# Performance work log

Measured on AMD Instinct MI355X. Metric: run time of the kernel, lower is better.

The kernel has to match this reference:

```python
import jax, jax.numpy as jnp
import numpy as np

H_GRID = 24
W_GRID = 24
NUM_HEADS = 3
FEAT_DIM = 192
HEAD_DIM = FEAT_DIM // NUM_HEADS  # 64
SCALE = HEAD_DIM ** -0.5
LN_EPS = 1e-5


def _positional():
    # matches get_positional_encodings with intrinsics=None; depends only on grid
    ys = jnp.linspace(-1.0, 1.0, H_GRID)
    xs = jnp.linspace(-1.0, 1.0, W_GRID)
    p3 = jnp.tile(ys, W_GRID)            # [N]
    p4 = jnp.repeat(xs, H_GRID)          # [N]
    p2 = p3 * p4
    p1 = p4 * p4
    p0 = p3 * p3
    return jnp.stack([p0, p1, p2, p3, p4, jnp.ones_like(p0)], axis=1)  # [N, 6]


def _layernorm(x, w, b):
    mu = jnp.mean(x, axis=-1, keepdims=True)
    var = jnp.mean((x - mu) ** 2, axis=-1, keepdims=True)
    return (x - mu) / jnp.sqrt(var + LN_EPS) * w + b


def _qkv_heads(x, qkv_w):
    # x: [B, N, C] -> q,k,v each [B, H, N, hd]
    B, N, _ = x.shape
    qkv = x @ qkv_w.T                                    # [B, N, 3*F]
    qkv = qkv.reshape(B, N, 3, NUM_HEADS, HEAD_DIM)
    qkv = jnp.transpose(qkv, (2, 0, 3, 1, 4))            # [3, B, H, N, hd]
    return qkv[0], qkv[1], qkv[2]


def _dual_softmax(attn):
    return jax.nn.softmax(attn, axis=-1) * jax.nn.softmax(attn, axis=-2)


def setup_inputs() -> dict:
    key = jax.random.key(0)
    ks = jax.random.split(key, 4)
    B, C = 64, 256
    in_dim, out_dim = C, 512
    dim_size = 2 * NUM_HEADS * (HEAD_DIM + 6) * (HEAD_DIM + 6)  # 29400
    return {
        "x1": jax.random.normal(ks[0], (B, C, H_GRID, W_GRID), jnp.float32),
        "x2": jax.random.normal(ks[1], (B, C, H_GRID, W_GRID), jnp.float32),
        "ln_w": jnp.ones((in_dim,), jnp.float32),
        "ln_b": jnp.zeros((in_dim,), jnp.float32),
        "qkv_w": jax.random.normal(ks[2], (3 * FEAT_DIM, in_dim), jnp.float32) * (in_dim ** -0.5),
        "proj_w": jax.random.normal(ks[3], (out_dim, dim_size), jnp.float32) * (dim_size ** -0.5),
        "proj_b": jnp.zeros((out_dim,), jnp.float32),
    }


def reference(x1, x2, ln_w, ln_b, qkv_w, proj_w, proj_b):
    B, C, h, w = x1.shape
    N = h * w
    x1t = _layernorm(x1.reshape(B, C, N).transpose(0, 2, 1), ln_w, ln_b)  # [B, N, C]
    x2t = _layernorm(x2.reshape(B, C, N).transpose(0, 2, 1), ln_w, ln_b)

    q1, k1, v1 = _qkv_heads(x1t, qkv_w)
    q2, k2, v2 = _qkv_heads(x2t, qkv_w)

    attn_1 = jnp.einsum("bhnd,bhmd->bhnm", q2, k1) * SCALE
    attn_2 = jnp.einsum("bhnd,bhmd->bhnm", q1, k2) * SCALE
    af1 = _dual_softmax(attn_1)
    af2 = _dual_softmax(attn_2)

    pos = jnp.broadcast_to(_positional(), (B, NUM_HEADS, N, 6))
    v1p = jnp.concatenate([v1, pos], axis=-1)  # [B, H, N, hd+6]
    v2p = jnp.concatenate([v2, pos], axis=-1)

    f1 = jnp.einsum("bhnd,bhnm,bhme->bhde", v1p, af1, v1p)  # [B, H, hd+6, hd+6]
    f2 = jnp.einsum("bhnd,bhnm,bhme->bhde", v2p, af2, v2p)

    feat = jnp.concatenate([f1.reshape(B, -1), f2.reshape(B, -1)], axis=-1)
    return jax.nn.relu(feat @ proj_w.T + proj_b)
```

## Files before the change

kernel.cpp:

```cpp
#include <hip/hip_runtime.h>

#define NSEQ 576
#define CDIM 256
#define HEADS 3
#define HD 64
#define FEAT 192
#define QKVF 576
#define QK_F 384
#define VP 70
#define BHN 192
#define DIMSZ 29400

typedef __attribute__((ext_vector_type(8))) _Float16 half8;
typedef __attribute__((ext_vector_type(4))) _Float16 half4;
typedef __attribute__((ext_vector_type(4))) float f32x4;

#define MFMA16(A,B,C) __builtin_amdgcn_mfma_f32_16x16x32_f16(A,B,C,0,0,0)

__device__ __forceinline__ float posval(int n, int pe){
  int yi = n % 24, xi = n / 24;
  float py = (float)yi * (2.0f/23.0f) - 1.0f;
  float px = (float)xi * (2.0f/23.0f) - 1.0f;
  switch(pe){
    case 0: return py*py;
    case 1: return px*px;
    case 2: return py*px;
    case 3: return py;
    case 4: return px;
    default: return 1.0f;
  }
}

template<int LD>
__device__ __forceinline__ half8 fragT(const _Float16 (*s)[LD], int row, int dbase){
  half4 a = *(const half4*)&s[row][dbase];
  half4 b = *(const half4*)&s[row][dbase + 16];
  return __builtin_shufflevector(a, b, 0, 1, 2, 3, 4, 5, 6, 7);
}

__device__ __forceinline__ void stage_copy64(const _Float16* __restrict__ src, int rstr,
                                             _Float16 (*d)[72], int t){
  #pragma unroll
  for (int k2 = 0; k2 < 2; ++k2){
    int idx = t + 256 * k2;
    int row = idx >> 3, c = (idx & 7) << 3;
    half8 v = *(const half8*)(src + (size_t)row * rstr + c);
    *(half4*)&d[row][c]     = (half4){v[0], v[1], v[2], v[3]};
    *(half4*)&d[row][c + 4] = (half4){v[4], v[5], v[6], v[7]};
  }
}

__device__ __forceinline__ int rotIdx(int row, int c16){
  return row * 64 + ((((c16) + row) & 7) << 3);
}

__global__ __launch_bounds__(192) void k_ln_stats(const float* __restrict__ x1, const float* __restrict__ x2,
                                                  float* __restrict__ mu, float* __restrict__ rstd){
  int idx = blockIdx.x;
  int i2 = idx / 192;
  int rem = idx % 192;
  int b = rem / 3, ng = rem % 3;
  int n = ng * 192 + threadIdx.x;
  const float* x = i2 ? x2 : x1;
  const float* xb = x + (size_t)b * CDIM * NSEQ + n;
  float s = 0.f, sq = 0.f;
  for (int c = 0; c < CDIM; ++c){
    float v = xb[(size_t)c * NSEQ];
    s += v; sq += v * v;
  }
  float m = s * (1.0f/256.0f);
  float var = sq * (1.0f/256.0f) - m * m;
  int o = (i2 * 64 + b) * NSEQ + n;
  mu[o] = m;
  rstd[o] = rsqrtf(var + 1e-5f);
}

__global__ __launch_bounds__(256) void k_qkv_gemm_mfma(const float* __restrict__ x1, const float* __restrict__ x2,
                                                       const float* __restrict__ mu, const float* __restrict__ rstd,
                                                       const float* __restrict__ lnw, const float* __restrict__ lnb,
                                                       const float* __restrict__ qkvw,
                                                       _Float16* __restrict__ qh, _Float16* __restrict__ ql,
                                                       _Float16* __restrict__ vpTh, _Float16* __restrict__ vpTl){
  int wg = (blockIdx.x & 7) * 1296 + (blockIdx.x >> 3);
  int ft = wg % 9;
  int mt = wg / 9;
  int ibn = mt * 64;
  int i2 = ibn / (64 * NSEQ);
  int bn = ibn % (64 * NSEQ);
  int b  = bn / NSEQ;
  int n0 = bn % NSEQ;
  const float* x = i2 ? x2 : x1;
  const float* xb = x + (size_t)b * CDIM * NSEQ + n0;
  __shared__ __align__(16) _Float16 Xh[64][68];
  __shared__ __align__(16) _Float16 Xl[64][68];
  __shared__ __align__(16) _Float16 Wh[64][68];
  __shared__ __align__(16) _Float16 Wl[64][68];
  __shared__ float smu[64], srstd[64], slnw[256], slnb[256];
  int t = threadIdx.x;
  int w = t >> 6, lane = t & 63, tx = lane & 15, hi = lane >> 4;
  if (t < 64){ smu[t] = mu[ibn + t]; srstd[t] = rstd[ibn + t]; }
  slnw[t] = lnw[t]; slnb[t] = lnb[t];

  f32x4 acc[4];
  #pragma unroll
  for (int s = 0; s < 4; ++s) acc[s] = (f32x4){0.f, 0.f, 0.f, 0.f};

  int nA = t & 63, cg = t >> 6;
  int fr = t >> 2, cq = t & 3;
  for (int c0 = 0; c0 < CDIM; c0 += 64){
    __syncthreads();
    float mun = smu[nA], rsn = srstd[nA];
    #pragma unroll
    for (int rr = 0; rr < 16; ++rr){
      int c = cg * 16 + rr;
      float v = xb[(size_t)(c0 + c) * NSEQ + nA];
      float xv = (v - mun) * rsn * slnw[c0 + c] + slnb[c0 + c];
      _Float16 hh = (_Float16)xv;
      Xh[nA][c] = hh;
      Xl[nA][c] = (_Float16)(xv - (float)hh);
    }
    const float* wp = qkvw + (size_t)(ft * 64 + fr) * CDIM + c0 + cq * 16;
    #pragma unroll
    for (int rr = 0; rr < 4; ++rr){
      float4 wv = *(const float4*)(wp + rr * 4);
      half4 h, l;
      h.x = (_Float16)wv.x; l.x = (_Float16)(wv.x - (float)h.x);
      h.y = (_Float16)wv.y; l.y = (_Float16)(wv.y - (float)h.y);
      h.z = (_Float16)wv.z; l.z = (_Float16)(wv.z - (float)h.z);
      h.w = (_Float16)wv.w; l.w = (_Float16)(wv.w - (float)h.w);
      *(half4*)&Wh[fr][cq * 16 + rr * 4] = h;
      *(half4*)&Wl[fr][cq * 16 + rr * 4] = l;
    }
    __syncthreads();
    #pragma unroll
    for (int kc = 0; kc < 2; ++kc){
      half8 wh = fragT<68>(Wh, w * 16 + tx, kc * 32 + hi * 4);
      half8 wl = fragT<68>(Wl, w * 16 + tx, kc * 32 + hi * 4);
      #pragma unroll
      for (int s = 0; s < 4; ++s){
        half8 xh = fragT<68>(Xh, s * 16 + tx, kc * 32 + hi * 4);
        half8 xl = fragT<68>(Xl, s * 16 + tx, kc * 32 + hi * 4);
        acc[s] = MFMA16(xh, wh, acc[s]);
        acc[s] = MFMA16(xl, wh, acc[s]);
        acc[s] = MFMA16(xh, wl, acc[s]);
      }
    }
  }
  if (ft < 6){
    #pragma unroll
    for (int s = 0; s < 4; ++s)
      #pragma unroll
      for (int rr = 0; rr < 4; ++rr){
        float v = acc[s][rr];
        _Float16 hh = (_Float16)v;
        size_t o = (size_t)(ibn + s * 16 + hi * 4 + rr) * QK_F + ft * 64 + w * 16 + tx;
        qh[o] = hh;
        ql[o] = (_Float16)(v - (float)hh);
      }
  } else {
    __syncthreads();
    #pragma unroll
    for (int s = 0; s < 4; ++s)
      #pragma unroll
      for (int rr = 0; rr < 4; ++rr){
        float v = acc[s][rr];
        _Float16 hh = (_Float16)v;
        Xh[s * 16 + hi * 4 + rr][w * 16 + tx] = hh;
        Xl[s * 16 + hi * 4 + rr][w * 16 + tx] = (_Float16)(v - (float)hh);
      }
    __syncthreads();
    int mbg = i2 * 192 + b * 3 + (ft - 6);
    #pragma unroll
    for (int it = 0; it < 16; ++it){
      int d = (t >> 6) + it * 4;
      int n2 = t & 63;
      size_t o = ((size_t)mbg * 80 + d) * NSEQ + n0 + n2;
      vpTh[o] = Xh[n2][d];
      vpTl[o] = Xl[n2][d];
    }
  }
}

__global__ __launch_bounds__(256) void k_pos_fill(_Float16* __restrict__ vpTh, _Float16* __restrict__ vpTl){
  int idx = blockIdx.x * 256 + threadIdx.x;
  if (idx >= 384 * 16 * NSEQ) return;
  int n = idx % NSEQ;
  int r = idx / NSEQ;
  int row = 64 + (r & 15);
  int mb = r >> 4;
  float v = 0.f;
  int pe = row - 64;
  if (pe < 6) v = posval(n, pe);
  _Float16 hh = (_Float16)v;
  size_t o = ((size_t)mb * 80 + row) * NSEQ + n;
  vpTh[o] = hh;
  vpTl[o] = (_Float16)(v - (float)hh);
}

__global__ __launch_bounds__(256) void k_attn_stats_mfma(const _Float16* __restrict__ qh, const _Float16* __restrict__ ql,
                                                         float* __restrict__ rs, float* __restrict__ cs_part){
  int wg = (blockIdx.x & 7) * 432 + (blockIdx.x >> 3);
  int map = wg / (BHN * 9);
  int r   = wg % (BHN * 9);
  int bh = r / 9, nt = r % 9;
  int b = bh / 3, h = bh % 3;
  int qi = 1 - map, ki = map;
  int mb = map * BHN + bh;
  const _Float16* qbh = qh + (size_t)((qi * 64 + b) * NSEQ) * QK_F + h * HD;
  const _Float16* qbl = ql + (size_t)((qi * 64 + b) * NSEQ) * QK_F + h * HD;
  const _Float16* kbh = qh + (size_t)((ki * 64 + b) * NSEQ) * QK_F + FEAT + h * HD;
  const _Float16* kbl = ql + (size_t)((ki * 64 + b) * NSEQ) * QK_F + FEAT + h * HD;
  int n0 = nt * 64;
  __shared__ __align__(16) _Float16 Kh[64 * 64];
  __shared__ __align__(16) _Float16 Kl[64 * 64];
  __shared__ float rsLds[4][64];
  int t = threadIdx.x;
  int w = t >> 6, lane = t & 63, tx = lane & 15, hi = lane >> 4;

  for (int idx = t; idx < 1024; idx += 256){
    int a = idx >> 9, rc = idx & 511, row = rc >> 3, c16 = rc & 7;
    const _Float16* src = a ? qbl : qbh;
    _Float16* dst = a ? Kl : Kh;
    *(half8*)(dst + rotIdx(row, c16)) = *(const half8*)(src + (size_t)(n0 + row) * QK_F + c16 * 8);
  }
  __syncthreads();
  half8 qAh[4][2], qAl[4][2];
  #pragma unroll
  for (int s = 0; s < 4; ++s)
    #pragma unroll
    for (int kc = 0; kc < 2; ++kc){
      qAh[s][kc] = *(half8*)(Kh + rotIdx(s * 16 + tx, kc * 4 + hi));
      qAl[s][kc] = *(half8*)(Kl + rotIdx(s * 16 + tx, kc * 4 + hi));
    }

  float rsum[4][4] = {};
  for (int mt = 0; mt < 9; ++mt){
    int m0 = mt * 64;
    __syncthreads();
    for (int idx = t; idx < 1024; idx += 256){
      int a = idx >> 9, rc = idx & 511, row = rc >> 3, c16 = rc & 7;
      const _Float16* src = a ? kbl : kbh;
      _Float16* dst = a ? Kl : Kh;
      *(half8*)(dst + rotIdx(row, c16)) = *(const half8*)(src + (size_t)(m0 + row) * QK_F + c16 * 8);
    }
    __syncthreads();
    f32x4 acc[4];
    #pragma unroll
    for (int s = 0; s < 4; ++s) acc[s] = (f32x4){0.f, 0.f, 0.f, 0.f};
    #pragma unroll
    for (int kc = 0; kc < 2; ++kc){
      half8 kb8 = *(half8*)(Kh + rotIdx(w * 16 + tx, kc * 4 + hi));
      half8 kl8 = *(half8*)(Kl + rotIdx(w * 16 + tx, kc * 4 + hi));
      #pragma unroll
      for (int s = 0; s < 4; ++s){
        acc[s] = MFMA16(qAh[s][kc], kb8, acc[s]);
        acc[s] = MFMA16(qAl[s][kc], kb8, acc[s]);
        acc[s] = MFMA16(qAh[s][kc], kl8, acc[s]);
      }
    }
    float csum = 0.f;
    #pragma unroll
    for (int s = 0; s < 4; ++s)
      #pragma unroll
      for (int rr = 0; rr < 4; ++rr){
        float e = __expf(acc[s][rr] * 0.125f);
        rsum[s][rr] += e;
        csum += e;
      }
    csum += __shfl_xor(csum, 16);
    csum += __shfl_xor(csum, 32);
    if (lane < 16)
      cs_part[((size_t)mb * 9 + nt) * NSEQ + m0 + w * 16 + tx] = csum;
  }
  #pragma unroll
  for (int s = 0; s < 4; ++s)
    #pragma unroll
    for (int rr = 0; rr < 4; ++rr){
      float v = rsum[s][rr];
      v += __shfl_xor(v, 1);
      v += __shfl_xor(v, 2);
      v += __shfl_xor(v, 4);
      v += __shfl_xor(v, 8);
      if (tx == 0) rsLds[w][s * 16 + hi * 4 + rr] = v;
    }
  __syncthreads();
  if (t < 64)
    rs[(size_t)mb * NSEQ + n0 + t] = rsLds[0][t] + rsLds[1][t] + rsLds[2][t] + rsLds[3][t];
}

__global__ __launch_bounds__(256) void k_cs_reduce(const float* __restrict__ cs_part, float* __restrict__ cs){
  int tid = blockIdx.x * 256 + threadIdx.x;
  if (tid >= 2 * BHN * NSEQ) return;
  int mb = tid / NSEQ, m = tid % NSEQ;
  float s = 0.f;
  #pragma unroll
  for (int p = 0; p < 9; ++p)
    s += cs_part[((size_t)mb * 9 + p) * NSEQ + m];
  cs[tid] = s;
}

__global__ __launch_bounds__(256) void k_apply_mfma(const _Float16* __restrict__ qh, const _Float16* __restrict__ ql,
                                                    const _Float16* __restrict__ vpTh, const _Float16* __restrict__ vpTl,
                                                    const float* __restrict__ rs, const float* __restrict__ cs,
                                                    _Float16* __restrict__ tTh, _Float16* __restrict__ tTl, int map){
  int wg = (blockIdx.x & 7) * 216 + (blockIdx.x >> 3);
  int bh = wg / 9, nt = wg % 9;
  int b = bh / 3, h = bh % 3;
  int qi = 1 - map, ki = map;
  int mb = map * BHN + bh;
  const _Float16* qbh = qh + (size_t)((qi * 64 + b) * NSEQ) * QK_F + h * HD;
  const _Float16* qbl = ql + (size_t)((qi * 64 + b) * NSEQ) * QK_F + h * HD;
  const _Float16* kbh = qh + (size_t)((ki * 64 + b) * NSEQ) * QK_F + FEAT + h * HD;
  const _Float16* kbl = ql + (size_t)((ki * 64 + b) * NSEQ) * QK_F + FEAT + h * HD;
  const _Float16* vTh = vpTh + (size_t)mb * 80 * NSEQ;
  const _Float16* vTl = vpTl + (size_t)mb * 80 * NSEQ;
  int n0 = nt * 64;
  __shared__ __align__(16) _Float16 Ash[64][72];
  __shared__ __align__(16) _Float16 Asl[64][72];
  __shared__ __align__(16) _Float16 Vth[80][72];
  __shared__ __align__(16) _Float16 Vtl[80][72];
  __shared__ float cinv[64];
  int t = threadIdx.x;
  int w = t >> 6, lane = t & 63, tx = lane & 15, hi = lane >> 4;

  stage_copy64(qbh + (size_t)n0 * QK_F, QK_F, Ash, t);
  stage_copy64(qbl + (size_t)n0 * QK_F, QK_F, Asl, t);
  __syncthreads();
  half8 qB0h = fragT<72>(Ash, w * 16 + tx, 0 + hi * 4);
  half8 qB1h = fragT<72>(Ash, w * 16 + tx, 32 + hi * 4);
  half8 qB0l = fragT<72>(Asl, w * 16 + tx, 0 + hi * 4);
  half8 qB1l = fragT<72>(Asl, w * 16 + tx, 32 + hi * 4);
  float rinv = 1.0f / rs[(size_t)mb * NSEQ + n0 + w * 16 + tx];

  f32x4 tacc[5];
  #pragma unroll
  for (int et = 0; et < 5; ++et) tacc[et] = (f32x4){0.f, 0.f, 0.f, 0.f};

  for (int mt = 0; mt < 9; ++mt){
    int m0 = mt * 64;
    __syncthreads();
    stage_copy64(kbh + (size_t)m0 * QK_F, QK_F, Ash, t);
    stage_copy64(kbl + (size_t)m0 * QK_F, QK_F, Asl, t);
    #pragma unroll
    for (int k2 = 0; k2 < 3; ++k2){
      int idx = t + 256 * k2;
      if (idx < 640){
        int row = idx >> 3, c = (idx & 7) << 3;
        half8 v1 = *(const half8*)(vTh + (size_t)row * NSEQ + m0 + c);
        *(half4*)&Vth[row][c]     = (half4){v1[0], v1[1], v1[2], v1[3]};
        *(half4*)&Vth[row][c + 4] = (half4){v1[4], v1[5], v1[6], v1[7]};
        half8 v2 = *(const half8*)(vTl + (size_t)row * NSEQ + m0 + c);
        *(half4*)&Vtl[row][c]     = (half4){v2[0], v2[1], v2[2], v2[3]};
        *(half4*)&Vtl[row][c + 4] = (half4){v2[4], v2[5], v2[6], v2[7]};
      }
    }
    if (t < 64) cinv[t] = 1.0f / cs[(size_t)mb * NSEQ + m0 + t];
    __syncthreads();

    f32x4 acc[4];
    #pragma unroll
    for (int s = 0; s < 4; ++s) acc[s] = (f32x4){0.f, 0.f, 0.f, 0.f};
    #pragma unroll
    for (int s = 0; s < 4; ++s){
      half8 kh0 = fragT<72>(Ash, s * 16 + tx, 0 + hi * 4);
      half8 kl0 = fragT<72>(Asl, s * 16 + tx, 0 + hi * 4);
      half8 kh1 = fragT<72>(Ash, s * 16 + tx, 32 + hi * 4);
      half8 kl1 = fragT<72>(Asl, s * 16 + tx, 32 + hi * 4);
      acc[s] = MFMA16(kh0, qB0h, acc[s]);
      acc[s] = MFMA16(kl0, qB0h, acc[s]);
      acc[s] = MFMA16(kh0, qB0l, acc[s]);
      acc[s] = MFMA16(kh1, qB1h, acc[s]);
      acc[s] = MFMA16(kl1, qB1h, acc[s]);
      acc[s] = MFMA16(kh1, qB1l, acc[s]);
    }
    half8 bph[2], bpl[2];
    #pragma unroll
    for (int s = 0; s < 4; ++s){
      #pragma unroll
      for (int rr = 0; rr < 4; ++rr){
        float af = __expf(acc[s][rr] * 0.25f) * rinv * cinv[s * 16 + hi * 4 + rr];
        _Float16 hh = (_Float16)af;
        bph[s >> 1][(s & 1) * 4 + rr] = hh;
        bpl[s >> 1][(s & 1) * 4 + rr] = (_Float16)(af - (float)hh);
      }
    }
    #pragma unroll
    for (int et = 0; et < 5; ++et)
      #pragma unroll
      for (int mc = 0; mc < 2; ++mc){
        half8 vhf = fragT<72>(Vth, et * 16 + tx, mc * 32 + hi * 4);
        half8 vlf = fragT<72>(Vtl, et * 16 + tx, mc * 32 + hi * 4);
        tacc[et] = MFMA16(vhf, bph[mc], tacc[et]);
        tacc[et] = MFMA16(vhf, bpl[mc], tacc[et]);
        tacc[et] = MFMA16(vlf, bph[mc], tacc[et]);
      }
  }
  #pragma unroll
  for (int et = 0; et < 5; ++et)
    #pragma unroll
    for (int rr = 0; rr < 4; ++rr){
      int e = et * 16 + hi * 4 + rr;
      float v = tacc[et][rr];
      _Float16 hh = (_Float16)v;
      size_t o = ((size_t)bh * 80 + e) * NSEQ + n0 + w * 16 + tx;
      tTh[o] = hh;
      tTl[o] = (_Float16)(v - (float)hh);
    }
}

__global__ __launch_bounds__(256) void k_f_gemm_mfma(const _Float16* __restrict__ vpTh, const _Float16* __restrict__ vpTl,
                                                     const _Float16* __restrict__ tTh, const _Float16* __restrict__ tTl,
                                                     float* __restrict__ featT3, int map){
  int wg = blockIdx.x;
  int mbL = wg / 3, part = wg % 3;
  int b = mbL / 3, h = mbL % 3;
  __shared__ __align__(16) _Float16 Ah[80][40], Al[80][40], Bh[80][40], Bl[80][40];
  int t = threadIdx.x;
  int w4 = t >> 6, lane = t & 63, tx = lane & 15, hi = lane >> 4;
  const _Float16* Abh = vpTh + (size_t)(map * BHN + mbL) * 80 * NSEQ;
  const _Float16* Abl = vpTl + (size_t)(map * BHN + mbL) * 80 * NSEQ;
  const _Float16* Bbh = tTh + (size_t)mbL * 80 * NSEQ;
  const _Float16* Bbl = tTl + (size_t)mbL * 80 * NSEQ;
  f32x4 acc[7];
  #pragma unroll
  for (int j = 0; j < 7; ++j) acc[j] = (f32x4){0.f, 0.f, 0.f, 0.f};

  for (int kc = part * 6; kc < part * 6 + 6; ++kc){
    int c0 = kc * 32;
    __syncthreads();
    #pragma unroll
    for (int k2 = 0; k2 < 2; ++k2){
      int idx = t + 256 * k2;
      if (idx < 320){
        int row = idx >> 2, cc = (idx & 3) << 3;
        *(half8*)&Ah[row][cc] = *(const half8*)(Abh + (size_t)row * NSEQ + c0 + cc);
        *(half8*)&Al[row][cc] = *(const half8*)(Abl + (size_t)row * NSEQ + c0 + cc);
        *(half8*)&Bh[row][cc] = *(const half8*)(Bbh + (size_t)row * NSEQ + c0 + cc);
        *(half8*)&Bl[row][cc] = *(const half8*)(Bbl + (size_t)row * NSEQ + c0 + cc);
      }
    }
    __syncthreads();
    #pragma unroll
    for (int j = 0; j < 7; ++j){
      int ti = w4 + 4 * j;
      if (ti < 25){
        int db = ti / 5, eb = ti % 5;
        half8 ah = *(const half8*)&Ah[db * 16 + tx][hi * 8];
        half8 al = *(const half8*)&Al[db * 16 + tx][hi * 8];
        half8 bh = *(const half8*)&Bh[eb * 16 + tx][hi * 8];
        half8 bl = *(const half8*)&Bl[eb * 16 + tx][hi * 8];
        acc[j] = MFMA16(ah, bh, acc[j]);
        acc[j] = MFMA16(al, bh, acc[j]);
        acc[j] = MFMA16(ah, bl, acc[j]);
      }
    }
  }
  #pragma unroll
  for (int j = 0; j < 7; ++j){
    int ti = w4 + 4 * j;
    if (ti < 25){
      int db = ti / 5, eb = ti % 5;
      #pragma unroll
      for (int rr = 0; rr < 4; ++rr){
        int d = db * 16 + hi * 4 + rr, e = eb * 16 + tx;
        if (d < VP && e < VP)
          featT3[(size_t)part * 1881600 + (size_t)(map * 14700 + h * 4900 + d * VP + e) * 64 + b] = acc[j][rr];
      }
    }
  }
}

__global__ __launch_bounds__(256) void k_feat_reduce(const float* __restrict__ featT3, float* __restrict__ featT){
  int gid = blockIdx.x * 256 + threadIdx.x;
  if (gid >= DIMSZ * 64) return;
  featT[gid] = featT3[gid] + featT3[1881600 + gid] + featT3[2 * 1881600 + gid];
}

__global__ __launch_bounds__(256) void k_proj_gemm(const float* __restrict__ featT, const float* __restrict__ pw,
                                                   float* __restrict__ p){
  int ot = blockIdx.x & 7;
  int s  = blockIdx.x >> 3;
  int o0 = ot * 64;
  int kbase = s * 300;
  __shared__ __align__(16) float As[20][72];
  __shared__ __align__(16) float Bs[20][72];
  int t = threadIdx.x, tx = t & 15, ty = t >> 4;
  float acc[4][4] = {};
  for (int kt = 0; kt < 15; ++kt){
    int k0 = kbase + kt * 20;
    __syncthreads();
    #pragma unroll
    for (int r = 0; r < 5; ++r){
      int idx = t + 256 * r;
      int bb = idx & 63, kk = idx >> 6;
      As[kk][bb] = featT[(size_t)(k0 + kk) * 64 + bb];
      int ko = idx % 20, oo = idx / 20;
      Bs[ko][oo] = pw[(size_t)(o0 + oo) * DIMSZ + k0 + ko];
    }
    __syncthreads();
    #pragma unroll
    for (int k = 0; k < 20; ++k){
      float4 a4 = *(const float4*)&As[k][ty * 4];
      float4 b4 = *(const float4*)&Bs[k][tx * 4];
      float aa[4] = {a4.x, a4.y, a4.z, a4.w};
      float bb[4] = {b4.x, b4.y, b4.z, b4.w};
      #pragma unroll
      for (int i = 0; i < 4; ++i)
        #pragma unroll
        for (int j = 0; j < 4; ++j)
          acc[i][j] += aa[i] * bb[j];
    }
  }
  int slice = s * 8 + ot;
  #pragma unroll
  for (int i = 0; i < 4; ++i){
    float4 st = make_float4(acc[i][0], acc[i][1], acc[i][2], acc[i][3]);
    *(float4*)&p[(size_t)slice * 4096 + (ty * 4 + i) * 64 + tx * 4] = st;
  }
}

__global__ __launch_bounds__(256) void k_finalize(const float* __restrict__ p, const float* __restrict__ pb,
                                                  float* __restrict__ out){
  int gid = blockIdx.x * 256 + threadIdx.x;
  int o = gid & 511, b = gid >> 9;
  int ot = o >> 6, lo = o & 63;
  float s = pb[o];
  for (int s2 = 0; s2 < 98; ++s2)
    s += p[(size_t)(s2 * 8 + ot) * 4096 + b * 64 + lo];
  out[gid] = fmaxf(s, 0.0f);
}

extern "C" void kernel_launch(void* const* d_in, const int* in_sizes, int n_in,
                              void* d_out, int out_size, void* d_ws, size_t ws_size,
                              hipStream_t stream) {
  const float* x1   = (const float*)d_in[0];
  const float* x2   = (const float*)d_in[1];
  const float* lnw  = (const float*)d_in[2];
  const float* lnb  = (const float*)d_in[3];
  const float* qkvw = (const float*)d_in[4];
  const float* pw   = (const float*)d_in[5];
  const float* pb   = (const float*)d_in[6];
  float* out = (float*)d_out;

  float* w = (float*)d_ws;
  float*     mu      = w;
  float*     rstd    = w + 73728;
  _Float16*  qh      = (_Float16*)(w + 147456);
  _Float16*  ql      = (_Float16*)(w + 14303232);
  _Float16*  vpTh    = (_Float16*)(w + 28459008);
  _Float16*  vpTl    = (_Float16*)(w + 37306368);
  _Float16*  tTh     = (_Float16*)(w + 46153728);
  _Float16*  tTl     = (_Float16*)(w + 50577408);
  float*     cs_part = w + 55001088;
  float*     featT   = w + 55001088;
  float*     rs      = w + 56991744;
  float*     cs      = w + 57212928;
  float*     featT3  = w + 57434112;
  float*     p       = w + 57434112;

  k_ln_stats<<<384, 192, 0, stream>>>(x1, x2, mu, rstd);
  k_qkv_gemm_mfma<<<10368, 256, 0, stream>>>(x1, x2, mu, rstd, lnw, lnb, qkvw, qh, ql, vpTh, vpTl);
  k_pos_fill<<<13824, 256, 0, stream>>>(vpTh, vpTl);
  k_attn_stats_mfma<<<3456, 256, 0, stream>>>(qh, ql, rs, cs_part);
  k_cs_reduce<<<864, 256, 0, stream>>>(cs_part, cs);
  for (int map = 0; map < 2; ++map){
    k_apply_mfma<<<1728, 256, 0, stream>>>(qh, ql, vpTh, vpTl, rs, cs, tTh, tTl, map);
    k_f_gemm_mfma<<<576, 256, 0, stream>>>(vpTh, vpTl, tTh, tTl, featT3, map);
  }
  k_feat_reduce<<<7350, 256, 0, stream>>>(featT3, featT);
  k_proj_gemm<<<784, 256, 0, stream>>>(featT, pw, p);
  k_finalize<<<128, 256, 0, stream>>>(p, pb, out);
}
```

Before: 757.0 us.

## Pre-split QKV weights to fp16 and compute three feature tiles per block

A new kernel converts the QKV weight matrix into fp16 high/low halves once per call. The QKV GEMM then reads weight fragments straight from global memory instead of staging them through shared memory. Each block now computes three 64-wide feature tiles, so the layernormed X tile is built once and reused across them, with a third as many blocks launched. The cost is more accumulator registers per thread, uncoalesced global weight loads, and one extra small kernel launch.

Result: slower. 781.7 us (+3.3%).

```diff
diff --git a/kernel.cpp b/kernel.cpp
--- a/kernel.cpp
+++ b/kernel.cpp
@@ -35,6 +35,12 @@
 __device__ __forceinline__ half8 fragT(const _Float16 (*s)[LD], int row, int dbase){
   half4 a = *(const half4*)&s[row][dbase];
   half4 b = *(const half4*)&s[row][dbase + 16];
+  return __builtin_shufflevector(a, b, 0, 1, 2, 3, 4, 5, 6, 7);
+}
+
+__device__ __forceinline__ half8 fragG(const _Float16* __restrict__ p){
+  half4 a = *(const half4*)p;
+  half4 b = *(const half4*)(p + 16);
   return __builtin_shufflevector(a, b, 0, 1, 2, 3, 4, 5, 6, 7);
 }
 
@@ -75,15 +81,25 @@
   rstd[o] = rsqrtf(var + 1e-5f);
 }
 
+__global__ __launch_bounds__(256) void k_w_split(const float* __restrict__ qkvw,
+                                                 _Float16* __restrict__ wsh, _Float16* __restrict__ wsl){
+  int f = blockIdx.x;
+  int c = threadIdx.x;
+  float v = qkvw[(size_t)f * CDIM + c];
+  _Float16 hh = (_Float16)v;
+  wsh[(size_t)f * CDIM + c] = hh;
+  wsl[(size_t)f * CDIM + c] = (_Float16)(v - (float)hh);
+}
+
 __global__ __launch_bounds__(256) void k_qkv_gemm_mfma(const float* __restrict__ x1, const float* __restrict__ x2,
                                                        const float* __restrict__ mu, const float* __restrict__ rstd,
                                                        const float* __restrict__ lnw, const float* __restrict__ lnb,
-                                                       const float* __restrict__ qkvw,
+                                                       const _Float16* __restrict__ wsh, const _Float16* __restrict__ wsl,
                                                        _Float16* __restrict__ qh, _Float16* __restrict__ ql,
                                                        _Float16* __restrict__ vpTh, _Float16* __restrict__ vpTl){
-  int wg = (blockIdx.x & 7) * 1296 + (blockIdx.x >> 3);
-  int ft = wg % 9;
-  int mt = wg / 9;
+  int wg = (blockIdx.x & 7) * 432 + (blockIdx.x >> 3);
+  int ftg = wg % 3;
+  int mt = wg / 3;
   int ibn = mt * 64;
   int i2 = ibn / (64 * NSEQ);
   int bn = ibn % (64 * NSEQ);
@@ -93,20 +109,19 @@
   const float* xb = x + (size_t)b * CDIM * NSEQ + n0;
   __shared__ __align__(16) _Float16 Xh[64][68];
   __shared__ __align__(16) _Float16 Xl[64][68];
-  __shared__ __align__(16) _Float16 Wh[64][68];
-  __shared__ __align__(16) _Float16 Wl[64][68];
   __shared__ float smu[64], srstd[64], slnw[256], slnb[256];
   int t = threadIdx.x;
   int w = t >> 6, lane = t & 63, tx = lane & 15, hi = lane >> 4;
   if (t < 64){ smu[t] = mu[ibn + t]; srstd[t] = rstd[ibn + t]; }
   slnw[t] = lnw[t]; slnb[t] = lnb[t];
 
-  f32x4 acc[4];
-  #pragma unroll
-  for (int s = 0; s < 4; ++s) acc[s] = (f32x4){0.f, 0.f, 0.f, 0.f};
+  f32x4 acc[3][4];
+  #pragma unroll
+  for (int f3 = 0; f3 < 3; ++f3)
+    #pragma unroll
+    for (int s = 0; s < 4; ++s) acc[f3][s] = (f32x4){0.f, 0.f, 0.f, 0.f};
 
   int nA = t & 63, cg = t >> 6;
-  int fr = t >> 2, cq = t & 3;
   for (int c0 = 0; c0 < CDIM; c0 += 64){
     __syncthreads();
     float mun = smu[nA], rsn = srstd[nA];
@@ -119,64 +134,67 @@
       Xh[nA][c] = hh;
       Xl[nA][c] = (_Float16)(xv - (float)hh);
     }
-    const float* wp = qkvw + (size_t)(ft * 64 + fr) * CDIM + c0 + cq * 16;
-    #pragma unroll
-    for (int rr = 0; rr < 4; ++rr){
-      float4 wv = *(const float4*)(wp + rr * 4);
-      half4 h, l;
-      h.x = (_Float16)wv.x; l.x = (_Float16)(wv.x - (float)h.x);
-      h.y = (_Float16)wv.y; l.y = (_Float16)(wv.y - (float)h.y);
-      h.z = (_Float16)wv.z; l.z = (_Float16)(wv.z - (float)h.z);
-      h.w = (_Float16)wv.w; l.w = (_Float16)(wv.w - (float)h.w);
-      *(half4*)&Wh[fr][cq * 16 + rr * 4] = h;
-      *(half4*)&Wl[fr][cq * 16 + rr * 4] = l;
-    }
     __syncthreads();
     #pragma unroll
     for (int kc = 0; kc < 2; ++kc){
-      half8 wh = fragT<68>(Wh, w * 16 + tx, kc * 32 + hi * 4);
-      half8 wl = fragT<68>(Wl, w * 16 + tx, kc * 32 + hi * 4);
+      half8 xh[4], xl[4];
       #pragma unroll
       for (int s = 0; s < 4; ++s){
-        half8 xh = fragT<68>(Xh, s * 16 + tx, kc * 32 + hi * 4);
-        half8 xl = fragT<68>(Xl, s * 16 + tx, kc * 32 + hi * 4);
-        acc[s] = MFMA16(xh, wh, acc[s]);
-        acc[s] = MFMA16(xl, wh, acc[s]);
-        acc[s] = MFMA16(xh, wl, acc[s]);
-      }
-    }
-  }
-  if (ft < 6){
-    #pragma unroll
-    for (int s = 0; s < 4; ++s)
-      #pragma unroll
-      for (int rr = 0; rr < 4; ++rr){
-        float v = acc[s][rr];
-        _Float16 hh = (_Float16)v;
-        size_t o = (size_t)(ibn + s * 16 + hi * 4 + rr) * QK_F + ft * 64 + w * 16 + tx;
-        qh[o] = hh;
-        ql[o] = (_Float16)(v - (float)hh);
-      }
+        xh[s] = fragT<68>(Xh, s * 16 + tx, kc * 32 + hi * 4);
+        xl[s] = fragT<68>(Xl, s * 16 + tx, kc * 32 + hi * 4);
+      }
+      #pragma unroll
+      for (int ft3 = 0; ft3 < 3; ++ft3){
+        int f = (ftg * 3 + ft3) * 64 + w * 16 + tx;
+        half8 wfh = fragG(wsh + (size_t)f * CDIM + c0 + kc * 32 + hi * 4);
+        half8 wfl = fragG(wsl + (size_t)f * CDIM + c0 + kc * 32 + hi * 4);
+        #pragma unroll
+        for (int s = 0; s < 4; ++s){
+          acc[ft3][s] = MFMA16(xh[s], wfh, acc[ft3][s]);
+          acc[ft3][s] = MFMA16(xl[s], wfh, acc[ft3][s]);
+          acc[ft3][s] = MFMA16(xh[s], wfl, acc[ft3][s]);
+        }
+      }
+    }
+  }
+  if (ftg < 2){
+    #pragma unroll
+    for (int ft3 = 0; ft3 < 3; ++ft3){
+      int ft = ftg * 3 + ft3;
+      #pragma unroll
+      for (int s = 0; s < 4; ++s)
+        #pragma unroll
+        for (int rr = 0; rr < 4; ++rr){
+          float v = acc[ft3][s][rr];
+          _Float16 hh = (_Float16)v;
+          size_t o = (size_t)(ibn + s * 16 + hi * 4 + rr) * QK_F + ft * 64 + w * 16 + tx;
+          qh[o] = hh;
+          ql[o] = (_Float16)(v - (float)hh);
+        }
+    }
   } else {
-    __syncthreads();
-    #pragma unroll
-    for (int s = 0; s < 4; ++s)
-      #pragma unroll
-      for (int rr = 0; rr < 4; ++rr){
-        float v = acc[s][rr];
-        _Float16 hh = (_Float16)v;
-        Xh[s * 16 + hi * 4 + rr][w * 16 + tx] = hh;
-        Xl[s * 16 + hi * 4 + rr][w * 16 + tx] = (_Float16)(v - (float)hh);
-      }
-    __syncthreads();
-    int mbg = i2 * 192 + b * 3 + (ft - 6);
-    #pragma unroll
-    for (int it = 0; it < 16; ++it){
-      int d = (t >> 6) + it * 4;
-      int n2 = t & 63;
-      size_t o = ((size_t)mbg * 80 + d) * NSEQ + n0 + n2;
-      vpTh[o] = Xh[n2][d];
-      vpTl[o] = Xl[n2][d];
+    #pragma unroll
+    for (int ft3 = 0; ft3 < 3; ++ft3){
+      __syncthreads();
+      #pragma unroll
+      for (int s = 0; s < 4; ++s)
+        #pragma unroll
+        for (int rr = 0; rr < 4; ++rr){
+          float v = acc[ft3][s][rr];
+          _Float16 hh = (_Float16)v;
+          Xh[s * 16 + hi * 4 + rr][w * 16 + tx] = hh;
+          Xl[s * 16 + hi * 4 + rr][w * 16 + tx] = (_Float16)(v - (float)hh);
+        }
+      __syncthreads();
+      int mbg = i2 * 192 + b * 3 + ft3;
+      #pragma unroll
+      for (int it = 0; it < 16; ++it){
+        int d = (t >> 6) + it * 4;
+        int n2 = t & 63;
+        size_t o = ((size_t)mbg * 80 + d) * NSEQ + n0 + n2;
+        vpTh[o] = Xh[n2][d];
+        vpTl[o] = Xl[n2][d];
+      }
     }
   }
 }
@@ -557,9 +575,12 @@
   float*     cs      = w + 57212928;
   float*     featT3  = w + 57434112;
   float*     p       = w + 57434112;
+  _Float16*  wsh     = (_Float16*)(w + 60645376);
+  _Float16*  wsl     = (_Float16*)(w + 60719104);
 
   k_ln_stats<<<384, 192, 0, stream>>>(x1, x2, mu, rstd);
-  k_qkv_gemm_mfma<<<10368, 256, 0, stream>>>(x1, x2, mu, rstd, lnw, lnb, qkvw, qh, ql, vpTh, vpTl);
+  k_w_split<<<576, 256, 0, stream>>>(qkvw, wsh, wsl);
+  k_qkv_gemm_mfma<<<3456, 256, 0, stream>>>(x1, x2, mu, rstd, lnw, lnb, wsh, wsl, qh, ql, vpTh, vpTl);
   k_pos_fill<<<13824, 256, 0, stream>>>(vpTh, vpTl);
   k_attn_stats_mfma<<<3456, 256, 0, stream>>>(qh, ql, rs, cs_part);
   k_cs_reduce<<<864, 256, 0, stream>>>(cs_part, cs);
```
